# Optimization experiments

Hardware: AMD Instinct MI355X
Metric: run time of the kernel (lower is better)

The kernel has to match this reference:

```python
import jax, jax.numpy as jnp
import numpy as np

T, B, D, H = 32, 128, 256, 768
MAX_PONDER = 8
EPS = 0.01


def setup_inputs() -> dict:
    key = jax.random.key(0)
    ks = jax.random.split(key, 6)
    s = 1.0 / np.sqrt(H)
    return {
        "input_": jax.random.normal(ks[0], (T, B, D), jnp.float32),
        "W_ih": jax.random.uniform(ks[1], (H, D + 1), jnp.float32, -s, s),
        "W_hh": jax.random.uniform(ks[2], (H, H), jnp.float32, -s, s),
        "b_ih": jax.random.uniform(ks[3], (H,), jnp.float32, -s, s),
        "b_hh": jax.random.uniform(ks[4], (H,), jnp.float32, -s, s),
        "w_p": jax.random.uniform(ks[5], (H,), jnp.float32, -s, s),
        "b_p": jnp.ones((1,), jnp.float32),  # torch reset_parameters fills ponder bias with 1
    }


def reference(input_, W_ih, W_hh, b_ih, b_hh, w_p, b_p):
    T_, B_, D_ = input_.shape
    H_ = W_hh.shape[0]
    dt = input_.dtype
    hx0 = jnp.zeros((B_, H_), dt)

    def time_step(carry, x_t):
        hx, pcost = carry

        def ponder(c, _):
            hx_i, ah, ahx, sc, spc, mask, flag = c
            # input row with ponder flag (0 on first act step, 1 afterwards)
            x_in = jnp.concatenate([x_t, jnp.full((B_, 1), flag, dt)], axis=1)
            # ponder cost assigned for active rows before update
            spc = jnp.where(mask, -ah, spc)
            hx_new = jnp.tanh(x_in @ W_ih.T + b_ih + hx_i @ W_hh.T + b_hh)
            hx_i = jnp.where(mask[:, None], hx_new, hx_i)
            mf = mask.astype(dt)
            ahx = ahx + mf[:, None] * hx_new  # accum_hx += hx (as in source)
            h = jax.nn.sigmoid(hx_new @ w_p + b_p[0])
            ah2 = ah + mf * h
            p = h - jnp.maximum(ah2 - 1.0, 0.0)
            ahx = ahx + (mf * p)[:, None] * hx_new  # accum_hx += p*hx
            sc = sc + mf
            mask2 = ah2 < (1.0 - EPS)
            return (hx_i, ah2, ahx, sc, spc, mask2, jnp.ones((), dt)), None

        init = (hx,
                jnp.zeros((B_,), dt),           # accum_h
                jnp.zeros((B_, H_), dt),        # accum_hx
                jnp.zeros((B_,), dt),           # step_count
                jnp.zeros((B_,), dt),           # step_ponder_cost
                jnp.ones((B_,), bool),          # selector
                jnp.zeros((), dt))              # flag
        (hx_i, ah, ahx, sc, spc, mask, flag), _ = jax.lax.scan(
            ponder, init, None, length=MAX_PONDER)
        hx_out = ahx / sc[:, None]
        return (hx_out, pcost + spc), (hx_out, sc)

    (hx_last, pcost), (all_hx, steps) = jax.lax.scan(
        time_step, (hx0, jnp.zeros((B_,), dt)), input_)
    # all_hx: [T,B,H], hx: [1,B,H], ponder_cost: [B], ponder_times: [T,B]
    return all_hx, hx_last[None], pcost, steps
```

## Files before the change

kernel.cpp:

```cpp
#include <hip/hip_runtime.h>
#include <math.h>

#define TT 32
#define BB 128
#define DD 256
#define HH 768
#define MAXP 8

#define RG   8
#define RPG  16
#define CB   12
#define CS   64
#define NTH  256
#define NCH  24

#define OFF_LAST  ((size_t)TT * BB * HH)
#define OFF_PCOST (OFF_LAST + (size_t)BB * HH)
#define OFF_STEPS (OFF_PCOST + BB)

#define ASCOPE __HIP_MEMORY_SCOPE_AGENT

typedef __attribute__((ext_vector_type(8))) short s16x8;
typedef __attribute__((ext_vector_type(4))) float f32x4;
typedef unsigned long long ull;

static __device__ __forceinline__ unsigned short f2bf(float f) {
    unsigned u = __float_as_uint(f);
    u = (u + 0x7fffu + ((u >> 16) & 1u)) >> 16;
    return (unsigned short)u;
}
static __device__ __forceinline__ float bf2f(unsigned short h) {
    return __uint_as_float(((unsigned)h) << 16);
}

__launch_bounds__(NTH, 1)
__global__ void act_kernel(const float* __restrict__ x,
                           const float* __restrict__ Wih,
                           const float* __restrict__ Whh,
                           const float* __restrict__ bih,
                           const float* __restrict__ bhh,
                           const float* __restrict__ wpv,
                           const float* __restrict__ bp,
                           float* __restrict__ out,
                           unsigned* __restrict__ flags,
                           ull* __restrict__ hxe,
                           float* __restrict__ zpt)
{
    const int tid  = threadIdx.x;
    const int rg   = blockIdx.x & 7;
    const int cbk  = blockIdx.x >> 3;
    const int r0   = rg * RPG;
    const int c0   = cbk * CS;
    const int CT   = tid >> 6;
    const int lane = tid & 63;
    const int am   = lane & 15;
    const int aq   = lane >> 4;

    __shared__ s16x8 A_s[NCH * 64];
    __shared__ s16x8 WB_s[4 * 8 * 64];
    __shared__ s16x8 xA_s[8 * 64];
    __shared__ unsigned short hxn_s[RPG][72];
    __shared__ float zp4_s[RPG][4];
    __shared__ float zred_s[RPG][13];
    __shared__ float ah_s[RPG], spc_s[RPG], pc_s[RPG], w1p_s[RPG], sc_s[RPG], inv_s[RPG];
    __shared__ int   act_s[RPG];
    __shared__ int   nact_s;
    __shared__ float bias_s[CS], wflag_s[CS], wp_s[CS];
    __shared__ float bp_s;

    s16x8 Breg[NCH];
    {
        const float* wr = Whh + (size_t)(c0 + CT*16 + am) * HH + aq*8;
        for (int ch = 0; ch < NCH; ++ch) {
            float4 a0 = *(const float4*)(wr + ch*32);
            float4 a1 = *(const float4*)(wr + ch*32 + 4);
            union { s16x8 v; unsigned short e[8]; } u;
            u.e[0]=f2bf(a0.x); u.e[1]=f2bf(a0.y); u.e[2]=f2bf(a0.z); u.e[3]=f2bf(a0.w);
            u.e[4]=f2bf(a1.x); u.e[5]=f2bf(a1.y); u.e[6]=f2bf(a1.z); u.e[7]=f2bf(a1.w);
            Breg[ch] = u.v;
        }
    }
    for (int ch = 0; ch < 8; ++ch) {
        const float* wr = Wih + (size_t)(c0 + CT*16 + am) * (DD+1) + ch*32 + aq*8;
        union { s16x8 v; unsigned short e[8]; } u;
        #pragma unroll
        for (int j = 0; j < 8; ++j) u.e[j] = f2bf(wr[j]);
        WB_s[(CT*8 + ch)*64 + lane] = u.v;
    }
    if (tid < CS) {
        bias_s[tid]  = bih[c0+tid] + bhh[c0+tid];
        wflag_s[tid] = Wih[(size_t)(c0+tid)*(DD+1) + DD];
        wp_s[tid]    = wpv[c0+tid];
    }
    if (tid == 0) bp_s = bp[0];
    if (tid < RPG) pc_s[tid] = 0.f;
    {
        s16x8 z8 = {0,0,0,0,0,0,0,0};
        #pragma unroll
        for (int j = 0; j < 6; ++j) A_s[j*NTH + tid] = z8;
    }
    __syncthreads();

    float ahx[48];
    unsigned it = 0;

    for (int t = 0; t < TT; ++t) {
        #pragma unroll
        for (int j = 0; j < 2; ++j) {
            const int s = j*NTH + tid;
            const int ch = s >> 6;
            const float* xb = x + ((size_t)t*BB + r0 + am)*DD + ch*32 + aq*8;
            float4 a0 = *(const float4*)xb;
            float4 a1 = *(const float4*)(xb + 4);
            union { s16x8 v; unsigned short e[8]; } u;
            u.e[0]=f2bf(a0.x); u.e[1]=f2bf(a0.y); u.e[2]=f2bf(a0.z); u.e[3]=f2bf(a0.w);
            u.e[4]=f2bf(a1.x); u.e[5]=f2bf(a1.y); u.e[6]=f2bf(a1.z); u.e[7]=f2bf(a1.w);
            xA_s[s] = u.v;
        }
        if (tid < RPG) { ah_s[tid]=0.f; spc_s[tid]=0.f; sc_s[tid]=0.f; act_s[tid]=1; }
        #pragma unroll
        for (int qq = 0; qq < 48; ++qq) ahx[qq] = 0.f;
        __syncthreads();

        f32x4 xi;
        {
            f32x4 acc = {0.f,0.f,0.f,0.f};
            #pragma unroll
            for (int ch = 0; ch < 8; ++ch)
                acc = __builtin_amdgcn_mfma_f32_16x16x32_bf16(
                        xA_s[ch*64 + lane], WB_s[(CT*8 + ch)*64 + lane], acc, 0, 0, 0);
            const float bs = bias_s[CT*16 + am];
            xi[0]=acc[0]+bs; xi[1]=acc[1]+bs; xi[2]=acc[2]+bs; xi[3]=acc[3]+bs;
        }

        int pk = 0;
        for (;;) {
            const unsigned par = it & 1u;
            ull*   exch = hxe + (size_t)(rg*2 + par) * (NCH*64) * 2;
            float* zpb  = zpt + (size_t)(rg*2 + par) * (CB*16);

            f32x4 acc = xi;
            #pragma unroll
            for (int ch = 0; ch < NCH; ++ch)
                acc = __builtin_amdgcn_mfma_f32_16x16x32_bf16(
                        A_s[ch*64 + lane], Breg[ch], acc, 0, 0, 0);
            const float fl = pk ? wflag_s[CT*16 + am] : 0.f;
            #pragma unroll
            for (int r = 0; r < 4; ++r)
                hxn_s[aq*4 + r][CT*16 + am] = f2bf(tanhf(acc[r] + fl));
            __syncthreads();

            if (tid < 64) {
                const int r = tid >> 2, cq = tid & 3;
                float s = 0.f;
                #pragma unroll
                for (int i = 0; i < 16; ++i)
                    s += bf2f(hxn_s[r][cq*16 + i]) * wp_s[cq*16 + i];
                zp4_s[r][cq] = s;
            }
            __syncthreads();
            if (tid < RPG) {
                const float zp = zp4_s[tid][0] + zp4_s[tid][1] + zp4_s[tid][2] + zp4_s[tid][3];
                __hip_atomic_store(&zpb[cbk*16 + tid], zp, __ATOMIC_RELAXED, ASCOPE);
            }
            if (tid < 128) {
                const int chd = tid >> 6, l = tid & 63;
                const int pm = l & 15, pq = l >> 4;
                const int cbase = chd*32 + pq*8;
                const ull lo = *(const ull*)&hxn_s[pm][cbase];
                const ull hi = *(const ull*)&hxn_s[pm][cbase + 4];
                ull* dst = exch + (size_t)((2*cbk + chd)*64 + l)*2;
                __hip_atomic_store(dst,     lo, __ATOMIC_RELAXED, ASCOPE);
                __hip_atomic_store(dst + 1, hi, __ATOMIC_RELAXED, ASCOPE);
            }

            ++it;
            __syncthreads();
            if (tid < 64) {
                if (tid == 0)
                    __hip_atomic_store(&flags[rg*16 + cbk], it, __ATOMIC_RELAXED, ASCOPE);
                const int pi = tid % 12;
                unsigned v;
                do { v = __hip_atomic_load(&flags[rg*16 + pi], __ATOMIC_RELAXED, ASCOPE); }
                while (!__all((int)(v >= it)));
                __builtin_amdgcn_fence(__ATOMIC_ACQUIRE, "agent");
            }
            __syncthreads();

            ull nlo[6], nhi[6];
            #pragma unroll
            for (int j = 0; j < 6; ++j) {
                ull* src = exch + (size_t)(j*NTH + tid)*2;
                nlo[j] = __hip_atomic_load(src,     __ATOMIC_RELAXED, ASCOPE);
                nhi[j] = __hip_atomic_load(src + 1, __ATOMIC_RELAXED, ASCOPE);
            }
            if (tid < 192) {
                const int bb_ = tid >> 4, rr = tid & 15;
                zred_s[rr][bb_] = __hip_atomic_load(&zpb[bb_*16 + rr], __ATOMIC_RELAXED, ASCOPE);
            }
            __syncthreads();

            if (tid < RPG) {
                float w1p = 0.f;
                if (act_s[tid]) {
                    float z = 0.f;
                    #pragma unroll
                    for (int i2 = 0; i2 < CB; ++i2) z += zred_s[tid][i2];
                    const float h = 1.f / (1.f + expf(-(z + bp_s)));
                    spc_s[tid] = -ah_s[tid];
                    const float ah2 = ah_s[tid] + h;
                    const float p = h - fmaxf(ah2 - 1.f, 0.f);
                    w1p = 1.f + p;
                    sc_s[tid] += 1.f;
                    ah_s[tid] = ah2;
                    act_s[tid] = (ah2 < 0.99f) ? 1 : 0;
                }
                w1p_s[tid] = w1p;
            }
            __syncthreads();

            {
                const float w1 = w1p_s[am];
                const int   aa = act_s[am];
                #pragma unroll
                for (int j = 0; j < 6; ++j) {
                    const ull lo = nlo[j], hi = nhi[j];
                    #pragma unroll
                    for (int i = 0; i < 4; ++i) {
                        ahx[j*8 + i]     += w1 * bf2f((unsigned short)(lo >> (16*i)));
                        ahx[j*8 + 4 + i] += w1 * bf2f((unsigned short)(hi >> (16*i)));
                    }
                    if (aa) {
                        union { ull u[2]; s16x8 v; } cv; cv.u[0] = lo; cv.u[1] = hi;
                        A_s[j*NTH + tid] = cv.v;
                    }
                }
            }
            if (tid == 0) {
                int n = 0;
                #pragma unroll
                for (int r2 = 0; r2 < RPG; ++r2) n += act_s[r2];
                nact_s = n;
            }
            ++pk;
            __syncthreads();
            if (nact_s == 0 || pk == MAXP) break;
        }

        if (tid < RPG) {
            inv_s[tid] = 1.f / sc_s[tid];
            pc_s[tid] += spc_s[tid];
            if (cbk == 0) out[OFF_STEPS + (size_t)t*BB + r0 + tid] = sc_s[tid];
        }
        __syncthreads();
        {
            const float inv = inv_s[am];
            #pragma unroll
            for (int j = 0; j < 6; ++j) {
                const int ch = j*4 + CT;
                float o[8];
                #pragma unroll
                for (int i = 0; i < 8; ++i) o[i] = ahx[j*8 + i] * inv;
                union { s16x8 v; unsigned short e[8]; } u;
                #pragma unroll
                for (int i = 0; i < 8; ++i) u.e[i] = f2bf(o[i]);
                A_s[j*NTH + tid] = u.v;
                if (cbk == 0) {
                    float* op = out + ((size_t)t*BB + r0 + am)*HH + ch*32 + aq*8;
                    *(float4*)op       = make_float4(o[0], o[1], o[2], o[3]);
                    *(float4*)(op + 4) = make_float4(o[4], o[5], o[6], o[7]);
                    if (t == TT-1) {
                        float* lp = out + OFF_LAST + (size_t)(r0 + am)*HH + ch*32 + aq*8;
                        *(float4*)lp       = make_float4(o[0], o[1], o[2], o[3]);
                        *(float4*)(lp + 4) = make_float4(o[4], o[5], o[6], o[7]);
                    }
                }
            }
        }
        __syncthreads();
    }
    if (cbk == 0 && tid < RPG) out[OFF_PCOST + r0 + tid] = pc_s[tid];
}

extern "C" void kernel_launch(void* const* d_in, const int* in_sizes, int n_in,
                              void* d_out, int out_size, void* d_ws, size_t ws_size,
                              hipStream_t stream) {
    const float* x   = (const float*)d_in[0];
    const float* Wih = (const float*)d_in[1];
    const float* Whh = (const float*)d_in[2];
    const float* bih = (const float*)d_in[3];
    const float* bhh = (const float*)d_in[4];
    const float* wpv = (const float*)d_in[5];
    const float* bp  = (const float*)d_in[6];
    float* out = (float*)d_out;

    unsigned* flags = (unsigned*)d_ws;
    ull*      hxe   = (ull*)((char*)d_ws + 4096);
    float*    zpt   = (float*)((char*)d_ws + 4096 + (size_t)RG*2*NCH*64*16);

    hipMemsetAsync(d_ws, 0, 4096, stream);
    act_kernel<<<dim3(RG*CB), dim3(NTH), 0, stream>>>(
        x, Wih, Whh, bih, bhh, wpv, bp, out, flags, hxe, zpt);
}
```

Measured before the change: 398.1 us.

## Compute halting logit from exchanged hidden state locally, drop partial-sum exchange

Each block now computes the full halting dot product from the complete hidden state it already reads from the global exchange buffer, using the ponder weights kept in registers. This removes the separate global exchange of per-block partial sums and several block-wide barriers. Per-row halting state moves from shared memory into registers, and the active-row count comes from a wave ballot. The change also prefetches the next timestep's input into registers and splits the MFMA chains across two accumulators to shorten dependency latency. In exchange every block redundantly does the full dot product, and the flag store now uses release ordering.

```diff
diff --git a/kernel.cpp b/kernel.cpp
--- a/kernel.cpp
+++ b/kernel.cpp
@@ -43,14 +43,13 @@
                            const float* __restrict__ bp,
                            float* __restrict__ out,
                            unsigned* __restrict__ flags,
-                           ull* __restrict__ hxe,
-                           float* __restrict__ zpt)
+                           ull* __restrict__ hxe)
 {
     const int tid  = threadIdx.x;
-    const int rg   = blockIdx.x & 7;
-    const int cbk  = blockIdx.x >> 3;
-    const int r0   = rg * RPG;
-    const int c0   = cbk * CS;
+    const int g    = blockIdx.x & 7;
+    const int ib   = blockIdx.x >> 3;
+    const int r0   = g * RPG;
+    const int c0   = ib * CS;
     const int CT   = tid >> 6;
     const int lane = tid & 63;
     const int am   = lane & 15;
@@ -60,13 +59,8 @@
     __shared__ s16x8 WB_s[4 * 8 * 64];
     __shared__ s16x8 xA_s[8 * 64];
     __shared__ unsigned short hxn_s[RPG][72];
-    __shared__ float zp4_s[RPG][4];
-    __shared__ float zred_s[RPG][13];
-    __shared__ float ah_s[RPG], spc_s[RPG], pc_s[RPG], w1p_s[RPG], sc_s[RPG], inv_s[RPG];
-    __shared__ int   act_s[RPG];
-    __shared__ int   nact_s;
-    __shared__ float bias_s[CS], wflag_s[CS], wp_s[CS];
-    __shared__ float bp_s;
+    __shared__ float zw_s[4][20];
+    __shared__ float bias_s[CS], wflag_s[CS];
 
     s16x8 Breg[NCH];
     {
@@ -90,98 +84,105 @@
     if (tid < CS) {
         bias_s[tid]  = bih[c0+tid] + bhh[c0+tid];
         wflag_s[tid] = Wih[(size_t)(c0+tid)*(DD+1) + DD];
-        wp_s[tid]    = wpv[c0+tid];
-    }
-    if (tid == 0) bp_s = bp[0];
-    if (tid < RPG) pc_s[tid] = 0.f;
+    }
+    const float bpr = bp[0];
+    float wpreg[48];
+    #pragma unroll
+    for (int j = 0; j < 6; ++j)
+        #pragma unroll
+        for (int i = 0; i < 8; ++i)
+            wpreg[j*8+i] = wpv[(j*4 + CT)*32 + aq*8 + i];
     {
         s16x8 z8 = {0,0,0,0,0,0,0,0};
         #pragma unroll
         for (int j = 0; j < 6; ++j) A_s[j*NTH + tid] = z8;
     }
-    __syncthreads();
 
     float ahx[48];
     unsigned it = 0;
+    float ahR = 0.f, spcR = 0.f, scR = 0.f, pcR = 0.f;
+    int   actR = 1;
+
+    float4 xp0, xp1, xp2, xp3;
+    {
+        const float* xb = x + (size_t)(r0 + am)*DD;
+        xp0 = *(const float4*)(xb + CT*32 + aq*8);
+        xp1 = *(const float4*)(xb + CT*32 + aq*8 + 4);
+        xp2 = *(const float4*)(xb + (4+CT)*32 + aq*8);
+        xp3 = *(const float4*)(xb + (4+CT)*32 + aq*8 + 4);
+    }
+    __syncthreads();
 
     for (int t = 0; t < TT; ++t) {
-        #pragma unroll
-        for (int j = 0; j < 2; ++j) {
-            const int s = j*NTH + tid;
-            const int ch = s >> 6;
-            const float* xb = x + ((size_t)t*BB + r0 + am)*DD + ch*32 + aq*8;
-            float4 a0 = *(const float4*)xb;
-            float4 a1 = *(const float4*)(xb + 4);
+        {
             union { s16x8 v; unsigned short e[8]; } u;
-            u.e[0]=f2bf(a0.x); u.e[1]=f2bf(a0.y); u.e[2]=f2bf(a0.z); u.e[3]=f2bf(a0.w);
-            u.e[4]=f2bf(a1.x); u.e[5]=f2bf(a1.y); u.e[6]=f2bf(a1.z); u.e[7]=f2bf(a1.w);
-            xA_s[s] = u.v;
-        }
-        if (tid < RPG) { ah_s[tid]=0.f; spc_s[tid]=0.f; sc_s[tid]=0.f; act_s[tid]=1; }
-        #pragma unroll
-        for (int qq = 0; qq < 48; ++qq) ahx[qq] = 0.f;
+            u.e[0]=f2bf(xp0.x); u.e[1]=f2bf(xp0.y); u.e[2]=f2bf(xp0.z); u.e[3]=f2bf(xp0.w);
+            u.e[4]=f2bf(xp1.x); u.e[5]=f2bf(xp1.y); u.e[6]=f2bf(xp1.z); u.e[7]=f2bf(xp1.w);
+            xA_s[tid] = u.v;
+            u.e[0]=f2bf(xp2.x); u.e[1]=f2bf(xp2.y); u.e[2]=f2bf(xp2.z); u.e[3]=f2bf(xp2.w);
+            u.e[4]=f2bf(xp3.x); u.e[5]=f2bf(xp3.y); u.e[6]=f2bf(xp3.z); u.e[7]=f2bf(xp3.w);
+            xA_s[NTH + tid] = u.v;
+        }
+        ahR = 0.f; spcR = 0.f; scR = 0.f; actR = 1;
+        #pragma unroll
+        for (int q = 0; q < 48; ++q) ahx[q] = 0.f;
         __syncthreads();
 
         f32x4 xi;
         {
-            f32x4 acc = {0.f,0.f,0.f,0.f};
-            #pragma unroll
-            for (int ch = 0; ch < 8; ++ch)
-                acc = __builtin_amdgcn_mfma_f32_16x16x32_bf16(
-                        xA_s[ch*64 + lane], WB_s[(CT*8 + ch)*64 + lane], acc, 0, 0, 0);
+            f32x4 a0 = {0.f,0.f,0.f,0.f}, a1 = {0.f,0.f,0.f,0.f};
+            #pragma unroll
+            for (int ch = 0; ch < 8; ch += 2) {
+                a0 = __builtin_amdgcn_mfma_f32_16x16x32_bf16(
+                        xA_s[ch*64 + lane],     WB_s[(CT*8 + ch)*64 + lane],     a0, 0,0,0);
+                a1 = __builtin_amdgcn_mfma_f32_16x16x32_bf16(
+                        xA_s[(ch+1)*64 + lane], WB_s[(CT*8 + ch+1)*64 + lane],   a1, 0,0,0);
+            }
             const float bs = bias_s[CT*16 + am];
-            xi[0]=acc[0]+bs; xi[1]=acc[1]+bs; xi[2]=acc[2]+bs; xi[3]=acc[3]+bs;
+            xi[0]=a0[0]+a1[0]+bs; xi[1]=a0[1]+a1[1]+bs;
+            xi[2]=a0[2]+a1[2]+bs; xi[3]=a0[3]+a1[3]+bs;
+        }
+        if (t + 1 < TT) {
+            const float* xb = x + ((size_t)(t+1)*BB + r0 + am)*DD;
+            xp0 = *(const float4*)(xb + CT*32 + aq*8);
+            xp1 = *(const float4*)(xb + CT*32 + aq*8 + 4);
+            xp2 = *(const float4*)(xb + (4+CT)*32 + aq*8);
+            xp3 = *(const float4*)(xb + (4+CT)*32 + aq*8 + 4);
         }
 
         int pk = 0;
         for (;;) {
             const unsigned par = it & 1u;
-            ull*   exch = hxe + (size_t)(rg*2 + par) * (NCH*64) * 2;
-            float* zpb  = zpt + (size_t)(rg*2 + par) * (CB*16);
-
-            f32x4 acc = xi;
-            #pragma unroll
-            for (int ch = 0; ch < NCH; ++ch)
-                acc = __builtin_amdgcn_mfma_f32_16x16x32_bf16(
-                        A_s[ch*64 + lane], Breg[ch], acc, 0, 0, 0);
+            ull* exch = hxe + (size_t)(g*2 + par) * (NCH*64*2);
+
+            f32x4 a0 = xi, a1 = {0.f,0.f,0.f,0.f};
+            #pragma unroll
+            for (int ch = 0; ch < NCH; ch += 2) {
+                a0 = __builtin_amdgcn_mfma_f32_16x16x32_bf16(A_s[ch*64 + lane],     Breg[ch],   a0, 0,0,0);
+                a1 = __builtin_amdgcn_mfma_f32_16x16x32_bf16(A_s[(ch+1)*64 + lane], Breg[ch+1], a1, 0,0,0);
+            }
             const float fl = pk ? wflag_s[CT*16 + am] : 0.f;
             #pragma unroll
             for (int r = 0; r < 4; ++r)
-                hxn_s[aq*4 + r][CT*16 + am] = f2bf(tanhf(acc[r] + fl));
-            __syncthreads();
-
+                hxn_s[aq*4 + r][CT*16 + am] = f2bf(tanhf(a0[r] + a1[r] + fl));
+            __syncthreads();
+
+            {
+                const int u4  = tid >> 6, l = tid & 63;
+                const int chd = u4 >> 1, half = u4 & 1;
+                const int pm  = l & 15, pq = l >> 4;
+                const ull v = *(const ull*)&hxn_s[pm][chd*32 + pq*8 + half*4];
+                __hip_atomic_store(exch + ((size_t)((2*ib + chd)*64 + l)*2 + half),
+                                   v, __ATOMIC_RELAXED, ASCOPE);
+            }
+            ++it;
+            __syncthreads();
+            if (tid == 0)
+                __hip_atomic_store(&flags[g*16 + ib], it, __ATOMIC_RELEASE, ASCOPE);
             if (tid < 64) {
-                const int r = tid >> 2, cq = tid & 3;
-                float s = 0.f;
-                #pragma unroll
-                for (int i = 0; i < 16; ++i)
-                    s += bf2f(hxn_s[r][cq*16 + i]) * wp_s[cq*16 + i];
-                zp4_s[r][cq] = s;
-            }
-            __syncthreads();
-            if (tid < RPG) {
-                const float zp = zp4_s[tid][0] + zp4_s[tid][1] + zp4_s[tid][2] + zp4_s[tid][3];
-                __hip_atomic_store(&zpb[cbk*16 + tid], zp, __ATOMIC_RELAXED, ASCOPE);
-            }
-            if (tid < 128) {
-                const int chd = tid >> 6, l = tid & 63;
-                const int pm = l & 15, pq = l >> 4;
-                const int cbase = chd*32 + pq*8;
-                const ull lo = *(const ull*)&hxn_s[pm][cbase];
-                const ull hi = *(const ull*)&hxn_s[pm][cbase + 4];
-                ull* dst = exch + (size_t)((2*cbk + chd)*64 + l)*2;
-                __hip_atomic_store(dst,     lo, __ATOMIC_RELAXED, ASCOPE);
-                __hip_atomic_store(dst + 1, hi, __ATOMIC_RELAXED, ASCOPE);
-            }
-
-            ++it;
-            __syncthreads();
-            if (tid < 64) {
-                if (tid == 0)
-                    __hip_atomic_store(&flags[rg*16 + cbk], it, __ATOMIC_RELAXED, ASCOPE);
-                const int pi = tid % 12;
+                const unsigned* fa = &flags[g*16 + (tid % 12)];
                 unsigned v;
-                do { v = __hip_atomic_load(&flags[rg*16 + pi], __ATOMIC_RELAXED, ASCOPE); }
+                do { v = __hip_atomic_load(fa, __ATOMIC_RELAXED, ASCOPE); }
                 while (!__all((int)(v >= it)));
                 __builtin_amdgcn_fence(__ATOMIC_ACQUIRE, "agent");
             }
@@ -194,34 +195,36 @@
                 nlo[j] = __hip_atomic_load(src,     __ATOMIC_RELAXED, ASCOPE);
                 nhi[j] = __hip_atomic_load(src + 1, __ATOMIC_RELAXED, ASCOPE);
             }
-            if (tid < 192) {
-                const int bb_ = tid >> 4, rr = tid & 15;
-                zred_s[rr][bb_] = __hip_atomic_load(&zpb[bb_*16 + rr], __ATOMIC_RELAXED, ASCOPE);
-            }
-            __syncthreads();
-
-            if (tid < RPG) {
-                float w1p = 0.f;
-                if (act_s[tid]) {
-                    float z = 0.f;
-                    #pragma unroll
-                    for (int i2 = 0; i2 < CB; ++i2) z += zred_s[tid][i2];
-                    const float h = 1.f / (1.f + expf(-(z + bp_s)));
-                    spc_s[tid] = -ah_s[tid];
-                    const float ah2 = ah_s[tid] + h;
-                    const float p = h - fmaxf(ah2 - 1.f, 0.f);
-                    w1p = 1.f + p;
-                    sc_s[tid] += 1.f;
-                    ah_s[tid] = ah2;
-                    act_s[tid] = (ah2 < 0.99f) ? 1 : 0;
+
+            float zp = 0.f;
+            #pragma unroll
+            for (int j = 0; j < 6; ++j) {
+                const ull lo = nlo[j], hi = nhi[j];
+                #pragma unroll
+                for (int i = 0; i < 4; ++i) {
+                    zp += bf2f((unsigned short)(lo >> (16*i))) * wpreg[j*8 + i];
+                    zp += bf2f((unsigned short)(hi >> (16*i))) * wpreg[j*8 + 4 + i];
                 }
-                w1p_s[tid] = w1p;
-            }
-            __syncthreads();
-
-            {
-                const float w1 = w1p_s[am];
-                const int   aa = act_s[am];
+            }
+            zp += __shfl_xor(zp, 16);
+            zp += __shfl_xor(zp, 32);
+            if (lane < 16) zw_s[CT][lane] = zp;
+            __syncthreads();
+            const float z = ((zw_s[0][am] + zw_s[1][am]) + zw_s[2][am]) + zw_s[3][am];
+
+            float w1 = 0.f;
+            if (actR) {
+                const float h = 1.f / (1.f + expf(-(z + bpr)));
+                spcR = -ahR;
+                const float ah2 = ahR + h;
+                const float p = h - fmaxf(ah2 - 1.f, 0.f);
+                w1 = 1.f + p;
+                scR += 1.f;
+                ahR = ah2;
+                actR = (ah2 < 0.99f) ? 1 : 0;
+            }
+
+            if (w1 != 0.f) {
                 #pragma unroll
                 for (int j = 0; j < 6; ++j) {
                     const ull lo = nlo[j], hi = nhi[j];
@@ -230,56 +233,42 @@
                         ahx[j*8 + i]     += w1 * bf2f((unsigned short)(lo >> (16*i)));
                         ahx[j*8 + 4 + i] += w1 * bf2f((unsigned short)(hi >> (16*i)));
                     }
-                    if (aa) {
-                        union { ull u[2]; s16x8 v; } cv; cv.u[0] = lo; cv.u[1] = hi;
-                        A_s[j*NTH + tid] = cv.v;
-                    }
+                    union { ull u[2]; s16x8 v; } cv; cv.u[0] = lo; cv.u[1] = hi;
+                    A_s[j*NTH + tid] = cv.v;
                 }
             }
-            if (tid == 0) {
-                int n = 0;
-                #pragma unroll
-                for (int r2 = 0; r2 < RPG; ++r2) n += act_s[r2];
-                nact_s = n;
-            }
+            const int nact = (int)__popcll(__ballot(actR != 0) & 0xFFFFull);
             ++pk;
             __syncthreads();
-            if (nact_s == 0 || pk == MAXP) break;
-        }
-
-        if (tid < RPG) {
-            inv_s[tid] = 1.f / sc_s[tid];
-            pc_s[tid] += spc_s[tid];
-            if (cbk == 0) out[OFF_STEPS + (size_t)t*BB + r0 + tid] = sc_s[tid];
+            if (nact == 0 || pk == MAXP) break;
+        }
+
+        pcR += spcR;
+        const float inv = 1.f / scR;
+        if (ib == 0 && tid < 16) out[OFF_STEPS + (size_t)t*BB + r0 + tid] = scR;
+        #pragma unroll
+        for (int j = 0; j < 6; ++j) {
+            float o[8];
+            #pragma unroll
+            for (int i = 0; i < 8; ++i) o[i] = ahx[j*8 + i] * inv;
+            union { s16x8 v; unsigned short e[8]; } u;
+            #pragma unroll
+            for (int i = 0; i < 8; ++i) u.e[i] = f2bf(o[i]);
+            A_s[j*NTH + tid] = u.v;
+            if (ib == 0) {
+                float* op = out + ((size_t)t*BB + r0 + am)*HH + (j*4 + CT)*32 + aq*8;
+                *(float4*)op       = make_float4(o[0], o[1], o[2], o[3]);
+                *(float4*)(op + 4) = make_float4(o[4], o[5], o[6], o[7]);
+                if (t == TT-1) {
+                    float* lp = out + OFF_LAST + (size_t)(r0 + am)*HH + (j*4 + CT)*32 + aq*8;
+                    *(float4*)lp       = make_float4(o[0], o[1], o[2], o[3]);
+                    *(float4*)(lp + 4) = make_float4(o[4], o[5], o[6], o[7]);
+                }
+            }
         }
         __syncthreads();
-        {
-            const float inv = inv_s[am];
-            #pragma unroll
-            for (int j = 0; j < 6; ++j) {
-                const int ch = j*4 + CT;
-                float o[8];
-                #pragma unroll
-                for (int i = 0; i < 8; ++i) o[i] = ahx[j*8 + i] * inv;
-                union { s16x8 v; unsigned short e[8]; } u;
-                #pragma unroll
-                for (int i = 0; i < 8; ++i) u.e[i] = f2bf(o[i]);
-                A_s[j*NTH + tid] = u.v;
-                if (cbk == 0) {
-                    float* op = out + ((size_t)t*BB + r0 + am)*HH + ch*32 + aq*8;
-                    *(float4*)op       = make_float4(o[0], o[1], o[2], o[3]);
-                    *(float4*)(op + 4) = make_float4(o[4], o[5], o[6], o[7]);
-                    if (t == TT-1) {
-                        float* lp = out + OFF_LAST + (size_t)(r0 + am)*HH + ch*32 + aq*8;
-                        *(float4*)lp       = make_float4(o[0], o[1], o[2], o[3]);
-                        *(float4*)(lp + 4) = make_float4(o[4], o[5], o[6], o[7]);
-                    }
-                }
-            }
-        }
-        __syncthreads();
-    }
-    if (cbk == 0 && tid < RPG) out[OFF_PCOST + r0 + tid] = pc_s[tid];
+    }
+    if (ib == 0 && tid < 16) out[OFF_PCOST + r0 + tid] = pcR;
 }
 
 extern "C" void kernel_launch(void* const* d_in, const int* in_sizes, int n_in,
@@ -296,9 +285,8 @@
 
     unsigned* flags = (unsigned*)d_ws;
     ull*      hxe   = (ull*)((char*)d_ws + 4096);
-    float*    zpt   = (float*)((char*)d_ws + 4096 + (size_t)RG*2*NCH*64*16);
 
     hipMemsetAsync(d_ws, 0, 4096, stream);
     act_kernel<<<dim3(RG*CB), dim3(NTH), 0, stream>>>(
-        x, Wih, Whh, bih, bhh, wpv, bp, out, flags, hxe, zpt);
-}
+        x, Wih, Whh, bih, bhh, wpv, bp, out, flags, hxe);
+}
```

Result: slower. 406.1 us (+2.0%).
